# Kernel tuning notes

Hardware: AMD Instinct MI355X
Metric: run time of the kernel (lower is better)

Reference implementation:

```python
import jax, jax.numpy as jnp
import numpy as np

B, L, D = 1, 512, 1024
NH, NKV, NR = 16, 4, 16
HD, RD = 64, 64
NREP = NH // NKV  # 4
ATTN_SCALE = 1.0 / float(np.sqrt(HD))
REL_SCALE = 1.0 / float(np.sqrt(RD))


def setup_inputs() -> dict:
    key = jax.random.key(0)
    ks = jax.random.split(key, 9)
    x = jax.random.normal(ks[0], (B, L, D), jnp.float32)
    symbols = jax.random.normal(ks[1], (B, L, D), jnp.float32)
    # standard llama-style RoPE frequencies: [L, HD//2]
    inv_freq = 1.0 / (10000.0 ** (np.arange(0, HD, 2, dtype=np.float32) / HD))
    f = np.outer(np.arange(L, dtype=np.float32), inv_freq)
    freqs_cos = jnp.asarray(np.cos(f), jnp.float32)
    freqs_sin = jnp.asarray(np.sin(f), jnp.float32)
    s = 0.02
    wq_attn = jax.random.normal(ks[2], (D, NH * HD), jnp.float32) * s
    wk_attn = jax.random.normal(ks[3], (D, NKV * HD), jnp.float32) * s
    wq_rel = jax.random.normal(ks[4], (D, NR * RD), jnp.float32) * s
    wk_rel = jax.random.normal(ks[5], (D, NR * RD), jnp.float32) * s
    wr = jax.random.normal(ks[6], (NR, NH * HD), jnp.float32) * s
    wv = jax.random.normal(ks[7], (D, NKV * HD), jnp.float32) * s
    wo = jax.random.normal(ks[8], (NH * HD, NH * HD), jnp.float32) * s
    return dict(x=x, symbols=symbols, freqs_cos=freqs_cos, freqs_sin=freqs_sin,
                wq_attn=wq_attn, wk_attn=wk_attn, wq_rel=wq_rel, wk_rel=wk_rel,
                wr=wr, wv=wv, wo=wo)


def _rope(t, cos, sin):
    # t: [b, l, h, hd]; cos/sin: [l, hd//2]
    tr = t.reshape(t.shape[:-1] + (HD // 2, 2))
    re, im = tr[..., 0], tr[..., 1]
    c = cos[None, :, None, :]
    s = sin[None, :, None, :]
    out = jnp.stack([re * c - im * s, re * s + im * c], axis=-1)
    return out.reshape(t.shape)


def reference(x, symbols, freqs_cos, freqs_sin, wq_attn, wk_attn, wq_rel, wk_rel, wr, wv, wo):
    b, l, _ = x.shape
    q = (x @ wq_attn).reshape(b, l, NH, HD)
    k = (x @ wk_attn).reshape(b, l, NKV, HD)
    qr = (x @ wq_rel).reshape(b, l, NR, RD)
    kr = (x @ wk_rel).reshape(b, l, NR, RD)
    sv = (symbols @ wv).reshape(b, l, NKV, HD)
    q = _rope(q, freqs_cos, freqs_sin)
    k = _rope(k, freqs_cos, freqs_sin)
    # GQA: repeat kv heads consecutively (matches torch repeat_kv expand+reshape)
    k = jnp.repeat(k, NREP, axis=2)
    sv = jnp.repeat(sv, NREP, axis=2)
    scores = jnp.einsum('bihd,bjhd->bhij', q, k) * ATTN_SCALE
    causal = jnp.tril(jnp.ones((l, l), bool))
    scores = jnp.where(causal[None, None], scores, -jnp.inf)
    attn = jax.nn.softmax(scores, axis=-1)  # [b, nh, l, l]
    # relation scores, identity activation, laid out as [b, i, j, nr]
    relations = jnp.einsum('bird,bjrd->bijr', qr, kr) * REL_SCALE
    proj_rel = (relations @ wr).reshape(b, l, l, NH, HD)  # dominant intermediate
    attended_symbols = jnp.einsum('bhij,bjhd->bihd', attn, sv)
    attended_relations = jnp.einsum('bhij,bijhd->bihd', attn, proj_rel)
    out = (attended_symbols + attended_relations).reshape(b, l, NH * HD) @ wo
    return out, attn, relations
```

## Files before the change

kernel.cpp:

```cpp
#include <hip/hip_runtime.h>
#include <math.h>

#define ATTN_SCALE 0.125f
#define REL_SCALE 0.125f

using ushort = unsigned short;
using bf16x8 = __attribute__((ext_vector_type(8))) __bf16;
using floatx4 = __attribute__((ext_vector_type(4))) float;
using ushort8 = __attribute__((ext_vector_type(8))) ushort;
using ushort4v = __attribute__((ext_vector_type(4))) ushort;

__device__ __forceinline__ ushort f2bf(float x) {
  unsigned int u = __builtin_bit_cast(unsigned int, x);
  u += 0x7fffu + ((u >> 16) & 1u);
  return (ushort)(u >> 16);
}

__device__ __forceinline__ void mfma_body(const ushort* __restrict__ A, int lda,
                                          const ushort* __restrict__ Bt, int ldb,
                                          int K, floatx4 (&acc)[2][2]) {
  __shared__ ushort As[64][72];
  __shared__ ushort Bs[64][72];
  const int tid = threadIdx.x;
  const int sr = tid >> 2, sc = (tid & 3) << 4;
  const int lane = tid & 63;
  const int wy = (tid >> 7) & 1, wx = (tid >> 6) & 1;
  const int lm = lane & 15, lq = lane >> 4;
  const ushort* a_rd = &As[32 * wy + lm][lq * 8];
  const ushort* b_rd = &Bs[32 * wx + lm][lq * 8];
  for (int k0 = 0; k0 < K; k0 += 64) {
    const ushort* Ap = A + (size_t)sr * lda + k0 + sc;
    ushort8 av0 = *(const ushort8*)Ap;
    ushort8 av1 = *(const ushort8*)(Ap + 8);
    const ushort* Bp = Bt + (size_t)sr * ldb + k0 + sc;
    ushort8 bv0 = *(const ushort8*)Bp;
    ushort8 bv1 = *(const ushort8*)(Bp + 8);
    __syncthreads();
    *(ushort8*)&As[sr][sc] = av0;
    *(ushort8*)&As[sr][sc + 8] = av1;
    *(ushort8*)&Bs[sr][sc] = bv0;
    *(ushort8*)&Bs[sr][sc + 8] = bv1;
    __syncthreads();
#pragma unroll
    for (int kh = 0; kh < 2; ++kh) {
      bf16x8 a0 = *(const bf16x8*)(a_rd + kh * 32);
      bf16x8 a1 = *(const bf16x8*)(a_rd + 16 * 72 + kh * 32);
      bf16x8 b0 = *(const bf16x8*)(b_rd + kh * 32);
      bf16x8 b1 = *(const bf16x8*)(b_rd + 16 * 72 + kh * 32);
      acc[0][0] = __builtin_amdgcn_mfma_f32_16x16x32_bf16(a0, b0, acc[0][0], 0, 0, 0);
      acc[0][1] = __builtin_amdgcn_mfma_f32_16x16x32_bf16(a0, b1, acc[0][1], 0, 0, 0);
      acc[1][0] = __builtin_amdgcn_mfma_f32_16x16x32_bf16(a1, b0, acc[1][0], 0, 0, 0);
      acc[1][1] = __builtin_amdgcn_mfma_f32_16x16x32_bf16(a1, b1, acc[1][1], 0, 0, 0);
    }
  }
}

#define EPILOG_VARS                                                   \
  const int lane = threadIdx.x & 63;                                  \
  const int wy = (threadIdx.x >> 7) & 1, wx = (threadIdx.x >> 6) & 1; \
  const int lm = lane & 15, lq = lane >> 4;

__global__ __launch_bounds__(256) void prep_kernel(
    const float* __restrict__ x, const float* __restrict__ sym,
    const float* __restrict__ wq, const float* __restrict__ wk,
    const float* __restrict__ wqr, const float* __restrict__ wkr,
    const float* __restrict__ wv, const float* __restrict__ wo,
    ushort* __restrict__ xb, ushort* __restrict__ symb,
    ushort* __restrict__ wqT, ushort* __restrict__ wkT, ushort* __restrict__ wqrT,
    ushort* __restrict__ wkrT, ushort* __restrict__ wvT, ushort* __restrict__ woT) {
  if (blockIdx.z == 6) {
    int b = blockIdx.y * 32 + blockIdx.x;
    if (b >= 512) return;
    int idx = b * 256 + threadIdx.x;
    int i4 = idx << 2;
    float4 v = *(const float4*)(x + i4);
    uint2 o;
    o.x = (unsigned)f2bf(v.x) | ((unsigned)f2bf(v.y) << 16);
    o.y = (unsigned)f2bf(v.z) | ((unsigned)f2bf(v.w) << 16);
    *(uint2*)(xb + i4) = o;
    float4 w = *(const float4*)(sym + i4);
    o.x = (unsigned)f2bf(w.x) | ((unsigned)f2bf(w.y) << 16);
    o.y = (unsigned)f2bf(w.z) | ((unsigned)f2bf(w.w) << 16);
    *(uint2*)(symb + i4) = o;
    return;
  }
  __shared__ ushort t[32][33];
  const float* in;
  ushort* out;
  int N;
  switch (blockIdx.z) {
    case 0: in = wq;  out = wqT;  N = 1024; break;
    case 1: in = wk;  out = wkT;  N = 256;  break;
    case 2: in = wqr; out = wqrT; N = 1024; break;
    case 3: in = wkr; out = wkrT; N = 1024; break;
    case 4: in = wv;  out = wvT;  N = 256;  break;
    default: in = wo; out = woT;  N = 1024; break;
  }
  int n0 = blockIdx.x << 5;
  if (n0 >= N) return;
  int k0 = blockIdx.y << 5;
  int tx = threadIdx.x & 31, ty = threadIdx.x >> 5;
#pragma unroll
  for (int rr = 0; rr < 32; rr += 8)
    t[ty + rr][tx] = f2bf(in[(size_t)(k0 + ty + rr) * N + n0 + tx]);
  __syncthreads();
#pragma unroll
  for (int rr = 0; rr < 32; rr += 8)
    out[(size_t)(n0 + ty + rr) * 1024 + k0 + tx] = t[tx][ty + rr];
}

__global__ __launch_bounds__(256) void proj_mfma(
    const ushort* __restrict__ xb, const ushort* __restrict__ symb,
    const ushort* __restrict__ wqT, const ushort* __restrict__ wkT,
    const ushort* __restrict__ wqrT, const ushort* __restrict__ wkrT,
    const ushort* __restrict__ wvT,
    ushort* __restrict__ qb, ushort* __restrict__ kb, ushort* __restrict__ qrb,
    ushort* __restrict__ krb, ushort* __restrict__ svT,
    const float* __restrict__ fcos, const float* __restrict__ fsin) {
  const int z = blockIdx.z;
  const ushort* A = xb;
  const ushort* Bt;
  ushort* C;
  int N;
  switch (z) {
    case 0: Bt = wqT;  C = qb;  N = 1024; break;
    case 1: Bt = wkT;  C = kb;  N = 256;  break;
    case 2: Bt = wqrT; C = qrb; N = 1024; break;
    case 3: Bt = wkrT; C = krb; N = 1024; break;
    default: A = symb; Bt = wvT; C = svT; N = 256; break;
  }
  const int bn = blockIdx.x << 6;
  if (bn >= N) return;
  const int bm = blockIdx.y << 6;
  floatx4 acc[2][2] = {};
  mfma_body(A + (size_t)bm * 1024, 1024, Bt + (size_t)bn * 1024, 1024, 1024, acc);
  EPILOG_VARS
  if (z <= 1) {
#pragma unroll
    for (int sy = 0; sy < 2; ++sy)
#pragma unroll
      for (int sx = 0; sx < 2; ++sx)
#pragma unroll
        for (int e = 0; e < 4; ++e) {
          int row = bm + 32 * wy + 16 * sy + 4 * lq + e;
          int col = bn + 32 * wx + 16 * sx + lm;
          float v = acc[sy][sx][e];
          float pv = __shfl_xor(v, 1);
          int d = col & 63, p = d >> 1;
          float c = fcos[(row << 5) + p], s = fsin[(row << 5) + p];
          float o = (d & 1) ? fmaf(pv, s, v * c) : fmaf(v, c, -pv * s);
          C[(size_t)row * N + col] = f2bf(o);
        }
  } else if (z == 4) {
#pragma unroll
    for (int sy = 0; sy < 2; ++sy)
#pragma unroll
      for (int sx = 0; sx < 2; ++sx)
#pragma unroll
        for (int e = 0; e < 4; ++e) {
          int row = bm + 32 * wy + 16 * sy + 4 * lq + e;
          int col = bn + 32 * wx + 16 * sx + lm;
          svT[(size_t)col * 512 + row] = f2bf(acc[sy][sx][e]);
        }
  } else {
#pragma unroll
    for (int sy = 0; sy < 2; ++sy)
#pragma unroll
      for (int sx = 0; sx < 2; ++sx)
#pragma unroll
        for (int e = 0; e < 4; ++e) {
          int row = bm + 32 * wy + 16 * sy + 4 * lq + e;
          int col = bn + 32 * wx + 16 * sx + lm;
          C[(size_t)row * N + col] = f2bf(acc[sy][sx][e]);
        }
  }
}

__global__ __launch_bounds__(256) void relflash_kernel(
    const ushort* __restrict__ qb, const ushort* __restrict__ kb,
    const ushort* __restrict__ svT, const ushort* __restrict__ qrb,
    const ushort* __restrict__ krb, float* __restrict__ attn,
    float* __restrict__ asym, float* __restrict__ rel) {
  __shared__ float S[16][516];
  __shared__ ushort P[16][520];
  const int bx = blockIdx.x;
  const int tid = threadIdx.x, wave = tid >> 6, lane = tid & 63;
  const int lm = lane & 15, lq = lane >> 4;
  if (bx >= 512) {
    const int b = bx - 512;
    const int bi0 = (b >> 4) << 5, bj0 = (b & 15) << 5;
    const int ib = bi0 + ((wave >> 1) << 4), jb = bj0 + ((wave & 1) << 4);
    const ushort* qrow = qrb + (size_t)(ib + lm) * 1024 + lq * 8;
    const ushort* krow = krb + (size_t)(jb + lm) * 1024 + lq * 8;
#pragma unroll
    for (int rq = 0; rq < 4; ++rq) {
      floatx4 acc[4];
#pragma unroll
      for (int rr = 0; rr < 4; ++rr) {
        int roff = ((rq << 2) + rr) << 6;
        bf16x8 a0 = *(const bf16x8*)(qrow + roff);
        bf16x8 a1 = *(const bf16x8*)(qrow + roff + 32);
        bf16x8 b0 = *(const bf16x8*)(krow + roff);
        bf16x8 b1 = *(const bf16x8*)(krow + roff + 32);
        floatx4 t = {0.f, 0.f, 0.f, 0.f};
        t = __builtin_amdgcn_mfma_f32_16x16x32_bf16(a0, b0, t, 0, 0, 0);
        t = __builtin_amdgcn_mfma_f32_16x16x32_bf16(a1, b1, t, 0, 0, 0);
        acc[rr] = t;
      }
#pragma unroll
      for (int e = 0; e < 4; ++e) {
        int i = ib + 4 * lq + e, j = jb + lm;
        float4 v = make_float4(acc[0][e] * REL_SCALE, acc[1][e] * REL_SCALE,
                               acc[2][e] * REL_SCALE, acc[3][e] * REL_SCALE);
        *(float4*)(rel + ((size_t)i * 512 + j) * 16 + (rq << 2)) = v;
      }
    }
    return;
  }
  const int h = bx >> 5, it = 31 - (bx & 31);
  const int i0 = it << 4, kv = h >> 2;
  const int ntiles = it + 1;
  const ushort* qrow = qb + (size_t)(i0 + lm) * 1024 + (h << 6) + lq * 8;
  bf16x8 a0 = *(const bf16x8*)(qrow);
  bf16x8 a1 = *(const bf16x8*)(qrow + 32);
  for (int jt = wave; jt < ntiles; jt += 4) {
    int jb = jt << 4;
    const ushort* krow = kb + (size_t)(jb + lm) * 256 + (kv << 6) + lq * 8;
    bf16x8 b0 = *(const bf16x8*)(krow);
    bf16x8 b1 = *(const bf16x8*)(krow + 32);
    floatx4 acc = {0.f, 0.f, 0.f, 0.f};
    acc = __builtin_amdgcn_mfma_f32_16x16x32_bf16(a0, b0, acc, 0, 0, 0);
    acc = __builtin_amdgcn_mfma_f32_16x16x32_bf16(a1, b1, acc, 0, 0, 0);
#pragma unroll
    for (int e = 0; e < 4; ++e) S[4 * lq + e][jb + lm] = acc[e] * ATTN_SCALE;
  }
  __syncthreads();
  const int row = tid >> 4, t16 = tid & 15;
  const int i = i0 + row;
  const int nj = ntiles << 4;
  float m = -INFINITY;
  for (int s = 0; (s << 6) < nj; ++s) {
    int j4 = (t16 << 2) + (s << 6);
    float4 v = *(const float4*)&S[row][j4];
    if (j4 + 0 <= i) m = fmaxf(m, v.x);
    if (j4 + 1 <= i) m = fmaxf(m, v.y);
    if (j4 + 2 <= i) m = fmaxf(m, v.z);
    if (j4 + 3 <= i) m = fmaxf(m, v.w);
  }
#pragma unroll
  for (int o = 8; o; o >>= 1) m = fmaxf(m, __shfl_xor(m, o, 16));
  float sum = 0.f;
  for (int s = 0; (s << 6) < nj; ++s) {
    int j4 = (t16 << 2) + (s << 6);
    float4 v = *(const float4*)&S[row][j4];
    if (j4 + 0 <= i) sum += __expf(v.x - m);
    if (j4 + 1 <= i) sum += __expf(v.y - m);
    if (j4 + 2 <= i) sum += __expf(v.z - m);
    if (j4 + 3 <= i) sum += __expf(v.w - m);
  }
#pragma unroll
  for (int o = 8; o; o >>= 1) sum += __shfl_xor(sum, o, 16);
  const float inv = 1.f / sum;
  float* arow = attn + (size_t)h * 262144 + (size_t)i * 512;
  for (int s = 0; s < 8; ++s) {
    int j4 = (t16 << 2) + (s << 6);
    float4 o4 = {0.f, 0.f, 0.f, 0.f};
    if (j4 < nj) {
      float4 v = *(const float4*)&S[row][j4];
      o4.x = (j4 + 0 <= i) ? __expf(v.x - m) * inv : 0.f;
      o4.y = (j4 + 1 <= i) ? __expf(v.y - m) * inv : 0.f;
      o4.z = (j4 + 2 <= i) ? __expf(v.z - m) * inv : 0.f;
      o4.w = (j4 + 3 <= i) ? __expf(v.w - m) * inv : 0.f;
    }
    *(float4*)(arow + j4) = o4;
    ushort4v p4;
    p4.x = f2bf(o4.x); p4.y = f2bf(o4.y); p4.z = f2bf(o4.z); p4.w = f2bf(o4.w);
    *(ushort4v*)&P[row][j4] = p4;
  }
  __syncthreads();
  const int dbase = wave << 4;
  floatx4 acc2 = {0.f, 0.f, 0.f, 0.f};
  const ushort* svrow = svT + (size_t)((kv << 6) + dbase + lm) * 512;
  const int kmax = (nj + 31) & ~31;
  for (int kt = 0; kt < kmax; kt += 32) {
    bf16x8 pa = *(const bf16x8*)&P[lm][kt + lq * 8];
    bf16x8 pb = *(const bf16x8*)(svrow + kt + lq * 8);
    acc2 = __builtin_amdgcn_mfma_f32_16x16x32_bf16(pa, pb, acc2, 0, 0, 0);
  }
#pragma unroll
  for (int e = 0; e < 4; ++e)
    asym[(size_t)(i0 + 4 * lq + e) * 1024 + (h << 6) + dbase + lm] = acc2[e];
}

__global__ __launch_bounds__(256) void tker_combine(const float* __restrict__ attn,
                                                    const float* __restrict__ rel,
                                                    const float* __restrict__ asym,
                                                    const float* __restrict__ wr,
                                                    ushort* __restrict__ attb) {
  const int i = blockIdx.x, tid = threadIdx.x;
  __shared__ float a_s[16][132];
  __shared__ float r_s[16][132];
  __shared__ float Ts[16][17];
  const int h = tid >> 4, r = tid & 15;
  float acc = 0.f;
  for (int j0 = 0; j0 <= i; j0 += 128) {
#pragma unroll
    for (int idx = tid; idx < 512; idx += 256) {
      int hh = idx >> 5, j4 = (idx & 31) << 2;
      *(float4*)&a_s[hh][j4] =
          *(const float4*)(attn + (size_t)hh * 262144 + (size_t)i * 512 + j0 + j4);
    }
#pragma unroll
    for (int idx = tid; idx < 512; idx += 256) {
      int j = idx >> 2, r4 = (idx & 3) << 2;
      float4 v = *(const float4*)(rel + ((size_t)i * 512 + j0 + j) * 16 + r4);
      r_s[r4 + 0][j] = v.x;
      r_s[r4 + 1][j] = v.y;
      r_s[r4 + 2][j] = v.z;
      r_s[r4 + 3][j] = v.w;
    }
    __syncthreads();
#pragma unroll
    for (int jj = 0; jj < 128; jj += 4) {
      float4 a4 = *(const float4*)&a_s[h][jj];
      float4 r4v = *(const float4*)&r_s[r][jj];
      acc = fmaf(a4.x, r4v.x, acc);
      acc = fmaf(a4.y, r4v.y, acc);
      acc = fmaf(a4.z, r4v.z, acc);
      acc = fmaf(a4.w, r4v.w, acc);
    }
    __syncthreads();
  }
  Ts[h][r] = acc;
  __syncthreads();
  const int hc = tid >> 4, d4 = (tid & 15) << 2;
  float4 o = *(const float4*)(asym + (size_t)i * 1024 + (hc << 6) + d4);
#pragma unroll
  for (int rr = 0; rr < 16; ++rr) {
    float tv = Ts[hc][rr];
    float4 w4 = *(const float4*)(wr + (size_t)rr * 1024 + (hc << 6) + d4);
    o.x = fmaf(tv, w4.x, o.x);
    o.y = fmaf(tv, w4.y, o.y);
    o.z = fmaf(tv, w4.z, o.z);
    o.w = fmaf(tv, w4.w, o.w);
  }
  ushort4v ob;
  ob.x = f2bf(o.x); ob.y = f2bf(o.y); ob.z = f2bf(o.z); ob.w = f2bf(o.w);
  *(ushort4v*)(attb + (size_t)i * 1024 + (hc << 6) + d4) = ob;
}

__global__ __launch_bounds__(256) void out_mfma(const ushort* __restrict__ attb,
                                                const ushort* __restrict__ woT,
                                                float* __restrict__ out) {
  __shared__ ushort As[64][72];
  __shared__ ushort Bs[32][72];
  const int bn = blockIdx.x << 5, bm = blockIdx.y << 6;
  const int tid = threadIdx.x;
  const int sr = tid >> 2, sc = (tid & 3) << 4;
  const int br = tid >> 3, bc = (tid & 7) << 3;
  const int lane = tid & 63;
  const int wy = (tid >> 7) & 1, wx = (tid >> 6) & 1;
  const int lm = lane & 15, lq = lane >> 4;
  const ushort* a_rd = &As[32 * wy + lm][lq * 8];
  const ushort* b_rd = &Bs[16 * wx + lm][lq * 8];
  floatx4 acc[2] = {};
  for (int k0 = 0; k0 < 1024; k0 += 64) {
    const ushort* Ap = attb + (size_t)(bm + sr) * 1024 + k0 + sc;
    ushort8 av0 = *(const ushort8*)Ap;
    ushort8 av1 = *(const ushort8*)(Ap + 8);
    ushort8 bv = *(const ushort8*)(woT + (size_t)(bn + br) * 1024 + k0 + bc);
    __syncthreads();
    *(ushort8*)&As[sr][sc] = av0;
    *(ushort8*)&As[sr][sc + 8] = av1;
    *(ushort8*)&Bs[br][bc] = bv;
    __syncthreads();
#pragma unroll
    for (int kh = 0; kh < 2; ++kh) {
      bf16x8 a0 = *(const bf16x8*)(a_rd + kh * 32);
      bf16x8 a1 = *(const bf16x8*)(a_rd + 16 * 72 + kh * 32);
      bf16x8 b0 = *(const bf16x8*)(b_rd + kh * 32);
      acc[0] = __builtin_amdgcn_mfma_f32_16x16x32_bf16(a0, b0, acc[0], 0, 0, 0);
      acc[1] = __builtin_amdgcn_mfma_f32_16x16x32_bf16(a1, b0, acc[1], 0, 0, 0);
    }
  }
#pragma unroll
  for (int sy = 0; sy < 2; ++sy)
#pragma unroll
    for (int e = 0; e < 4; ++e) {
      int row = bm + 32 * wy + 16 * sy + 4 * lq + e;
      int col = bn + 16 * wx + lm;
      out[(size_t)row * 1024 + col] = acc[sy][e];
    }
}

extern "C" void kernel_launch(void* const* d_in, const int* in_sizes, int n_in,
                              void* d_out, int out_size, void* d_ws, size_t ws_size,
                              hipStream_t stream) {
  const float* x       = (const float*)d_in[0];
  const float* symbols = (const float*)d_in[1];
  const float* fcos    = (const float*)d_in[2];
  const float* fsin    = (const float*)d_in[3];
  const float* wq_attn = (const float*)d_in[4];
  const float* wk_attn = (const float*)d_in[5];
  const float* wq_rel  = (const float*)d_in[6];
  const float* wk_rel  = (const float*)d_in[7];
  const float* wr      = (const float*)d_in[8];
  const float* wv      = (const float*)d_in[9];
  const float* wo      = (const float*)d_in[10];

  float* out  = (float*)d_out;
  float* attn = out + 524288;
  float* rel  = attn + 4194304;

  char* wsb = (char*)d_ws;
  const size_t MB = 1 << 20;
  ushort* xb   = (ushort*)(wsb);
  ushort* symb = (ushort*)(wsb + 1 * MB);
  ushort* wqT  = (ushort*)(wsb + 2 * MB);
  ushort* wkT  = (ushort*)(wsb + 4 * MB);
  ushort* wqrT = (ushort*)(wsb + 4 * MB + 512 * 1024);
  ushort* wkrT = (ushort*)(wsb + 6 * MB + 512 * 1024);
  ushort* wvT  = (ushort*)(wsb + 8 * MB + 512 * 1024);
  ushort* woT  = (ushort*)(wsb + 9 * MB);
  ushort* qb   = (ushort*)(wsb + 11 * MB);
  ushort* kb   = (ushort*)(wsb + 12 * MB);
  ushort* qrb  = (ushort*)(wsb + 12 * MB + 256 * 1024);
  ushort* krb  = (ushort*)(wsb + 13 * MB + 256 * 1024);
  ushort* svT  = (ushort*)(wsb + 14 * MB + 256 * 1024);
  float*  asym = (float*)(wsb + 2 * MB);
  ushort* attb = (ushort*)(wsb + 4 * MB + 512 * 1024);

  prep_kernel<<<dim3(32, 32, 7), 256, 0, stream>>>(x, symbols, wq_attn, wk_attn,
                                                   wq_rel, wk_rel, wv, wo,
                                                   xb, symb, wqT, wkT, wqrT, wkrT, wvT, woT);
  proj_mfma<<<dim3(16, 8, 5), 256, 0, stream>>>(xb, symb, wqT, wkT, wqrT, wkrT, wvT,
                                                qb, kb, qrb, krb, svT, fcos, fsin);
  relflash_kernel<<<dim3(768), 256, 0, stream>>>(qb, kb, svT, qrb, krb, attn, asym, rel);
  tker_combine<<<dim3(512), 256, 0, stream>>>(attn, rel, asym, wr, attb);
  out_mfma<<<dim3(32, 8), 256, 0, stream>>>(attb, woT, out);
}
```

Measured before the change: 153.8 us.

## Fuse fp32-to-bf16 conversion and weight transpose into GEMM loads; cache softmax exps

```diff
diff --git a/kernel.cpp b/kernel.cpp
--- a/kernel.cpp
+++ b/kernel.cpp
@@ -16,30 +16,64 @@
   return (ushort)(u >> 16);
 }
 
-__device__ __forceinline__ void mfma_body(const ushort* __restrict__ A, int lda,
-                                          const ushort* __restrict__ Bt, int ldb,
-                                          int K, floatx4 (&acc)[2][2]) {
+__global__ __launch_bounds__(256) void proj_mfma(
+    const float* __restrict__ x, const float* __restrict__ symbols,
+    const float* __restrict__ wq, const float* __restrict__ wk,
+    const float* __restrict__ wqr, const float* __restrict__ wkr,
+    const float* __restrict__ wv,
+    ushort* __restrict__ qb, ushort* __restrict__ kb, ushort* __restrict__ qrb,
+    ushort* __restrict__ krb, ushort* __restrict__ svT,
+    const float* __restrict__ fcos, const float* __restrict__ fsin) {
   __shared__ ushort As[64][72];
   __shared__ ushort Bs[64][72];
+  const int z = blockIdx.z;
+  const float* A = x;
+  const float* W;
+  ushort* C;
+  int N;
+  switch (z) {
+    case 0: W = wq;  C = qb;  N = 1024; break;
+    case 1: W = wk;  C = kb;  N = 256;  break;
+    case 2: W = wqr; C = qrb; N = 1024; break;
+    case 3: W = wkr; C = krb; N = 1024; break;
+    default: A = symbols; W = wv; C = svT; N = 256; break;
+  }
+  const int bn = blockIdx.x << 6;
+  if (bn >= N) return;
+  const int bm = blockIdx.y << 6;
   const int tid = threadIdx.x;
   const int sr = tid >> 2, sc = (tid & 3) << 4;
+  const int kk = tid >> 4, nl = (tid & 15) << 2;
   const int lane = tid & 63;
   const int wy = (tid >> 7) & 1, wx = (tid >> 6) & 1;
   const int lm = lane & 15, lq = lane >> 4;
   const ushort* a_rd = &As[32 * wy + lm][lq * 8];
   const ushort* b_rd = &Bs[32 * wx + lm][lq * 8];
-  for (int k0 = 0; k0 < K; k0 += 64) {
-    const ushort* Ap = A + (size_t)sr * lda + k0 + sc;
-    ushort8 av0 = *(const ushort8*)Ap;
-    ushort8 av1 = *(const ushort8*)(Ap + 8);
-    const ushort* Bp = Bt + (size_t)sr * ldb + k0 + sc;
-    ushort8 bv0 = *(const ushort8*)Bp;
-    ushort8 bv1 = *(const ushort8*)(Bp + 8);
+  floatx4 acc[2][2] = {};
+  for (int k0 = 0; k0 < 1024; k0 += 64) {
+    const float* Ap = A + (size_t)(bm + sr) * 1024 + k0 + sc;
+    float4 f0 = *(const float4*)(Ap);
+    float4 f1 = *(const float4*)(Ap + 4);
+    float4 f2 = *(const float4*)(Ap + 8);
+    float4 f3 = *(const float4*)(Ap + 12);
+    ushort8 av0 = ushort8{f2bf(f0.x), f2bf(f0.y), f2bf(f0.z), f2bf(f0.w),
+                          f2bf(f1.x), f2bf(f1.y), f2bf(f1.z), f2bf(f1.w)};
+    ushort8 av1 = ushort8{f2bf(f2.x), f2bf(f2.y), f2bf(f2.z), f2bf(f2.w),
+                          f2bf(f3.x), f2bf(f3.y), f2bf(f3.z), f2bf(f3.w)};
+    float4 bw[4];
+#pragma unroll
+    for (int p = 0; p < 4; ++p)
+      bw[p] = *(const float4*)(W + (size_t)(k0 + kk + 16 * p) * N + bn + nl);
     __syncthreads();
     *(ushort8*)&As[sr][sc] = av0;
     *(ushort8*)&As[sr][sc + 8] = av1;
-    *(ushort8*)&Bs[sr][sc] = bv0;
-    *(ushort8*)&Bs[sr][sc + 8] = bv1;
+#pragma unroll
+    for (int p = 0; p < 4; ++p) {
+      Bs[nl + 0][kk + 16 * p] = f2bf(bw[p].x);
+      Bs[nl + 1][kk + 16 * p] = f2bf(bw[p].y);
+      Bs[nl + 2][kk + 16 * p] = f2bf(bw[p].z);
+      Bs[nl + 3][kk + 16 * p] = f2bf(bw[p].w);
+    }
     __syncthreads();
 #pragma unroll
     for (int kh = 0; kh < 2; ++kh) {
@@ -53,88 +87,6 @@
       acc[1][1] = __builtin_amdgcn_mfma_f32_16x16x32_bf16(a1, b1, acc[1][1], 0, 0, 0);
     }
   }
-}
-
-#define EPILOG_VARS                                                   \
-  const int lane = threadIdx.x & 63;                                  \
-  const int wy = (threadIdx.x >> 7) & 1, wx = (threadIdx.x >> 6) & 1; \
-  const int lm = lane & 15, lq = lane >> 4;
-
-__global__ __launch_bounds__(256) void prep_kernel(
-    const float* __restrict__ x, const float* __restrict__ sym,
-    const float* __restrict__ wq, const float* __restrict__ wk,
-    const float* __restrict__ wqr, const float* __restrict__ wkr,
-    const float* __restrict__ wv, const float* __restrict__ wo,
-    ushort* __restrict__ xb, ushort* __restrict__ symb,
-    ushort* __restrict__ wqT, ushort* __restrict__ wkT, ushort* __restrict__ wqrT,
-    ushort* __restrict__ wkrT, ushort* __restrict__ wvT, ushort* __restrict__ woT) {
-  if (blockIdx.z == 6) {
-    int b = blockIdx.y * 32 + blockIdx.x;
-    if (b >= 512) return;
-    int idx = b * 256 + threadIdx.x;
-    int i4 = idx << 2;
-    float4 v = *(const float4*)(x + i4);
-    uint2 o;
-    o.x = (unsigned)f2bf(v.x) | ((unsigned)f2bf(v.y) << 16);
-    o.y = (unsigned)f2bf(v.z) | ((unsigned)f2bf(v.w) << 16);
-    *(uint2*)(xb + i4) = o;
-    float4 w = *(const float4*)(sym + i4);
-    o.x = (unsigned)f2bf(w.x) | ((unsigned)f2bf(w.y) << 16);
-    o.y = (unsigned)f2bf(w.z) | ((unsigned)f2bf(w.w) << 16);
-    *(uint2*)(symb + i4) = o;
-    return;
-  }
-  __shared__ ushort t[32][33];
-  const float* in;
-  ushort* out;
-  int N;
-  switch (blockIdx.z) {
-    case 0: in = wq;  out = wqT;  N = 1024; break;
-    case 1: in = wk;  out = wkT;  N = 256;  break;
-    case 2: in = wqr; out = wqrT; N = 1024; break;
-    case 3: in = wkr; out = wkrT; N = 1024; break;
-    case 4: in = wv;  out = wvT;  N = 256;  break;
-    default: in = wo; out = woT;  N = 1024; break;
-  }
-  int n0 = blockIdx.x << 5;
-  if (n0 >= N) return;
-  int k0 = blockIdx.y << 5;
-  int tx = threadIdx.x & 31, ty = threadIdx.x >> 5;
-#pragma unroll
-  for (int rr = 0; rr < 32; rr += 8)
-    t[ty + rr][tx] = f2bf(in[(size_t)(k0 + ty + rr) * N + n0 + tx]);
-  __syncthreads();
-#pragma unroll
-  for (int rr = 0; rr < 32; rr += 8)
-    out[(size_t)(n0 + ty + rr) * 1024 + k0 + tx] = t[tx][ty + rr];
-}
-
-__global__ __launch_bounds__(256) void proj_mfma(
-    const ushort* __restrict__ xb, const ushort* __restrict__ symb,
-    const ushort* __restrict__ wqT, const ushort* __restrict__ wkT,
-    const ushort* __restrict__ wqrT, const ushort* __restrict__ wkrT,
-    const ushort* __restrict__ wvT,
-    ushort* __restrict__ qb, ushort* __restrict__ kb, ushort* __restrict__ qrb,
-    ushort* __restrict__ krb, ushort* __restrict__ svT,
-    const float* __restrict__ fcos, const float* __restrict__ fsin) {
-  const int z = blockIdx.z;
-  const ushort* A = xb;
-  const ushort* Bt;
-  ushort* C;
-  int N;
-  switch (z) {
-    case 0: Bt = wqT;  C = qb;  N = 1024; break;
-    case 1: Bt = wkT;  C = kb;  N = 256;  break;
-    case 2: Bt = wqrT; C = qrb; N = 1024; break;
-    case 3: Bt = wkrT; C = krb; N = 1024; break;
-    default: A = symb; Bt = wvT; C = svT; N = 256; break;
-  }
-  const int bn = blockIdx.x << 6;
-  if (bn >= N) return;
-  const int bm = blockIdx.y << 6;
-  floatx4 acc[2][2] = {};
-  mfma_body(A + (size_t)bm * 1024, 1024, Bt + (size_t)bn * 1024, 1024, 1024, acc);
-  EPILOG_VARS
   if (z <= 1) {
 #pragma unroll
     for (int sy = 0; sy < 2; ++sy)
@@ -253,10 +205,12 @@
   for (int s = 0; (s << 6) < nj; ++s) {
     int j4 = (t16 << 2) + (s << 6);
     float4 v = *(const float4*)&S[row][j4];
-    if (j4 + 0 <= i) sum += __expf(v.x - m);
-    if (j4 + 1 <= i) sum += __expf(v.y - m);
-    if (j4 + 2 <= i) sum += __expf(v.z - m);
-    if (j4 + 3 <= i) sum += __expf(v.w - m);
+    v.x = (j4 + 0 <= i) ? __expf(v.x - m) : 0.f;
+    v.y = (j4 + 1 <= i) ? __expf(v.y - m) : 0.f;
+    v.z = (j4 + 2 <= i) ? __expf(v.z - m) : 0.f;
+    v.w = (j4 + 3 <= i) ? __expf(v.w - m) : 0.f;
+    sum += v.x + v.y + v.z + v.w;
+    *(float4*)&S[row][j4] = v;
   }
 #pragma unroll
   for (int o = 8; o; o >>= 1) sum += __shfl_xor(sum, o, 16);
@@ -267,10 +221,10 @@
     float4 o4 = {0.f, 0.f, 0.f, 0.f};
     if (j4 < nj) {
       float4 v = *(const float4*)&S[row][j4];
-      o4.x = (j4 + 0 <= i) ? __expf(v.x - m) * inv : 0.f;
-      o4.y = (j4 + 1 <= i) ? __expf(v.y - m) * inv : 0.f;
-      o4.z = (j4 + 2 <= i) ? __expf(v.z - m) * inv : 0.f;
-      o4.w = (j4 + 3 <= i) ? __expf(v.w - m) * inv : 0.f;
+      o4.x = v.x * inv;
+      o4.y = v.y * inv;
+      o4.z = v.z * inv;
+      o4.w = v.w * inv;
     }
     *(float4*)(arow + j4) = o4;
     ushort4v p4;
@@ -350,14 +304,14 @@
 }
 
 __global__ __launch_bounds__(256) void out_mfma(const ushort* __restrict__ attb,
-                                                const ushort* __restrict__ woT,
+                                                const float* __restrict__ wo,
                                                 float* __restrict__ out) {
   __shared__ ushort As[64][72];
   __shared__ ushort Bs[32][72];
   const int bn = blockIdx.x << 5, bm = blockIdx.y << 6;
   const int tid = threadIdx.x;
   const int sr = tid >> 2, sc = (tid & 3) << 4;
-  const int br = tid >> 3, bc = (tid & 7) << 3;
+  const int kk = tid >> 3, nl = (tid & 7) << 2;
   const int lane = tid & 63;
   const int wy = (tid >> 7) & 1, wx = (tid >> 6) & 1;
   const int lm = lane & 15, lq = lane >> 4;
@@ -368,11 +322,20 @@
     const ushort* Ap = attb + (size_t)(bm + sr) * 1024 + k0 + sc;
     ushort8 av0 = *(const ushort8*)Ap;
     ushort8 av1 = *(const ushort8*)(Ap + 8);
-    ushort8 bv = *(const ushort8*)(woT + (size_t)(bn + br) * 1024 + k0 + bc);
+    float4 bw[2];
+#pragma unroll
+    for (int p = 0; p < 2; ++p)
+      bw[p] = *(const float4*)(wo + (size_t)(k0 + kk + 32 * p) * 1024 + bn + nl);
     __syncthreads();
     *(ushort8*)&As[sr][sc] = av0;
     *(ushort8*)&As[sr][sc + 8] = av1;
-    *(ushort8*)&Bs[br][bc] = bv;
+#pragma unroll
+    for (int p = 0; p < 2; ++p) {
+      Bs[nl + 0][kk + 32 * p] = f2bf(bw[p].x);
+      Bs[nl + 1][kk + 32 * p] = f2bf(bw[p].y);
+      Bs[nl + 2][kk + 32 * p] = f2bf(bw[p].z);
+      Bs[nl + 3][kk + 32 * p] = f2bf(bw[p].w);
+    }
     __syncthreads();
 #pragma unroll
     for (int kh = 0; kh < 2; ++kh) {
@@ -413,29 +376,19 @@
   float* rel  = attn + 4194304;
 
   char* wsb = (char*)d_ws;
-  const size_t MB = 1 << 20;
-  ushort* xb   = (ushort*)(wsb);
-  ushort* symb = (ushort*)(wsb + 1 * MB);
-  ushort* wqT  = (ushort*)(wsb + 2 * MB);
-  ushort* wkT  = (ushort*)(wsb + 4 * MB);
-  ushort* wqrT = (ushort*)(wsb + 4 * MB + 512 * 1024);
-  ushort* wkrT = (ushort*)(wsb + 6 * MB + 512 * 1024);
-  ushort* wvT  = (ushort*)(wsb + 8 * MB + 512 * 1024);
-  ushort* woT  = (ushort*)(wsb + 9 * MB);
-  ushort* qb   = (ushort*)(wsb + 11 * MB);
-  ushort* kb   = (ushort*)(wsb + 12 * MB);
-  ushort* qrb  = (ushort*)(wsb + 12 * MB + 256 * 1024);
-  ushort* krb  = (ushort*)(wsb + 13 * MB + 256 * 1024);
-  ushort* svT  = (ushort*)(wsb + 14 * MB + 256 * 1024);
-  float*  asym = (float*)(wsb + 2 * MB);
-  ushort* attb = (ushort*)(wsb + 4 * MB + 512 * 1024);
-
-  prep_kernel<<<dim3(32, 32, 7), 256, 0, stream>>>(x, symbols, wq_attn, wk_attn,
-                                                   wq_rel, wk_rel, wv, wo,
-                                                   xb, symb, wqT, wkT, wqrT, wkrT, wvT, woT);
-  proj_mfma<<<dim3(16, 8, 5), 256, 0, stream>>>(xb, symb, wqT, wkT, wqrT, wkrT, wvT,
+  const size_t KB = 1024;
+  ushort* qb   = (ushort*)(wsb);
+  ushort* kb   = (ushort*)(wsb + 1024 * KB);
+  ushort* qrb  = (ushort*)(wsb + 1280 * KB);
+  ushort* krb  = (ushort*)(wsb + 2304 * KB);
+  ushort* svT  = (ushort*)(wsb + 3328 * KB);
+  float*  asym = (float*)(wsb + 3584 * KB);
+  ushort* attb = (ushort*)(wsb + 5632 * KB);
+
+  proj_mfma<<<dim3(16, 8, 5), 256, 0, stream>>>(x, symbols, wq_attn, wk_attn,
+                                                wq_rel, wk_rel, wv,
                                                 qb, kb, qrb, krb, svT, fcos, fsin);
   relflash_kernel<<<dim3(768), 256, 0, stream>>>(qb, kb, svT, qrb, krb, attn, asym, rel);
   tker_combine<<<dim3(512), 256, 0, stream>>>(attn, rel, asym, wr, attb);
-  out_mfma<<<dim3(32, 8), 256, 0, stream>>>(attb, woT, out);
-}
+  out_mfma<<<dim3(32, 8), 256, 0, stream>>>(attb, wo, out);
+}
```

Result: slower. 169.5 us (+10.2%).

## Compute attention-relation contraction with MFMA using transposed bf16 relation copy

Applied to the files above, without the earlier changes.

```diff
diff --git a/kernel.cpp b/kernel.cpp
--- a/kernel.cpp
+++ b/kernel.cpp
@@ -180,7 +180,8 @@
     const ushort* __restrict__ qb, const ushort* __restrict__ kb,
     const ushort* __restrict__ svT, const ushort* __restrict__ qrb,
     const ushort* __restrict__ krb, float* __restrict__ attn,
-    float* __restrict__ asym, float* __restrict__ rel) {
+    float* __restrict__ asym, float* __restrict__ rel,
+    ushort* __restrict__ rel_bT) {
   __shared__ float S[16][516];
   __shared__ ushort P[16][520];
   const int bx = blockIdx.x;
@@ -213,6 +214,11 @@
         float4 v = make_float4(acc[0][e] * REL_SCALE, acc[1][e] * REL_SCALE,
                                acc[2][e] * REL_SCALE, acc[3][e] * REL_SCALE);
         *(float4*)(rel + ((size_t)i * 512 + j) * 16 + (rq << 2)) = v;
+        size_t tb = (size_t)i * 8192 + (size_t)(rq << 2) * 512 + j;
+        rel_bT[tb]         = f2bf(v.x);
+        rel_bT[tb + 512]   = f2bf(v.y);
+        rel_bT[tb + 1024]  = f2bf(v.z);
+        rel_bT[tb + 1536]  = f2bf(v.w);
       }
     }
     return;
@@ -253,10 +259,12 @@
   for (int s = 0; (s << 6) < nj; ++s) {
     int j4 = (t16 << 2) + (s << 6);
     float4 v = *(const float4*)&S[row][j4];
-    if (j4 + 0 <= i) sum += __expf(v.x - m);
-    if (j4 + 1 <= i) sum += __expf(v.y - m);
-    if (j4 + 2 <= i) sum += __expf(v.z - m);
-    if (j4 + 3 <= i) sum += __expf(v.w - m);
+    v.x = (j4 + 0 <= i) ? __expf(v.x - m) : 0.f;
+    v.y = (j4 + 1 <= i) ? __expf(v.y - m) : 0.f;
+    v.z = (j4 + 2 <= i) ? __expf(v.z - m) : 0.f;
+    v.w = (j4 + 3 <= i) ? __expf(v.w - m) : 0.f;
+    sum += v.x + v.y + v.z + v.w;
+    *(float4*)&S[row][j4] = v;
   }
 #pragma unroll
   for (int o = 8; o; o >>= 1) sum += __shfl_xor(sum, o, 16);
@@ -267,10 +275,10 @@
     float4 o4 = {0.f, 0.f, 0.f, 0.f};
     if (j4 < nj) {
       float4 v = *(const float4*)&S[row][j4];
-      o4.x = (j4 + 0 <= i) ? __expf(v.x - m) * inv : 0.f;
-      o4.y = (j4 + 1 <= i) ? __expf(v.y - m) * inv : 0.f;
-      o4.z = (j4 + 2 <= i) ? __expf(v.z - m) * inv : 0.f;
-      o4.w = (j4 + 3 <= i) ? __expf(v.w - m) * inv : 0.f;
+      o4.x = v.x * inv;
+      o4.y = v.y * inv;
+      o4.z = v.z * inv;
+      o4.w = v.w * inv;
     }
     *(float4*)(arow + j4) = o4;
     ushort4v p4;
@@ -293,60 +301,56 @@
 }
 
 __global__ __launch_bounds__(256) void tker_combine(const float* __restrict__ attn,
-                                                    const float* __restrict__ rel,
+                                                    const ushort* __restrict__ rel_bT,
                                                     const float* __restrict__ asym,
                                                     const float* __restrict__ wr,
                                                     ushort* __restrict__ attb) {
-  const int i = blockIdx.x, tid = threadIdx.x;
-  __shared__ float a_s[16][132];
-  __shared__ float r_s[16][132];
-  __shared__ float Ts[16][17];
-  const int h = tid >> 4, r = tid & 15;
-  float acc = 0.f;
-  for (int j0 = 0; j0 <= i; j0 += 128) {
-#pragma unroll
-    for (int idx = tid; idx < 512; idx += 256) {
-      int hh = idx >> 5, j4 = (idx & 31) << 2;
-      *(float4*)&a_s[hh][j4] =
-          *(const float4*)(attn + (size_t)hh * 262144 + (size_t)i * 512 + j0 + j4);
-    }
-#pragma unroll
-    for (int idx = tid; idx < 512; idx += 256) {
-      int j = idx >> 2, r4 = (idx & 3) << 2;
-      float4 v = *(const float4*)(rel + ((size_t)i * 512 + j0 + j) * 16 + r4);
-      r_s[r4 + 0][j] = v.x;
-      r_s[r4 + 1][j] = v.y;
-      r_s[r4 + 2][j] = v.z;
-      r_s[r4 + 3][j] = v.w;
-    }
-    __syncthreads();
-#pragma unroll
-    for (int jj = 0; jj < 128; jj += 4) {
-      float4 a4 = *(const float4*)&a_s[h][jj];
-      float4 r4v = *(const float4*)&r_s[r][jj];
-      acc = fmaf(a4.x, r4v.x, acc);
-      acc = fmaf(a4.y, r4v.y, acc);
-      acc = fmaf(a4.z, r4v.z, acc);
-      acc = fmaf(a4.w, r4v.w, acc);
-    }
-    __syncthreads();
-  }
-  Ts[h][r] = acc;
+  const int i0 = blockIdx.x << 2;
+  const int tid = threadIdx.x, wave = tid >> 6, lane = tid & 63;
+  const int lm = lane & 15, lq = lane >> 4;
+  const int i = i0 + wave;
+  __shared__ float Ts[4][16][17];
+  floatx4 acc = {0.f, 0.f, 0.f, 0.f};
+  const float* arow = attn + (size_t)lm * 262144 + (size_t)i * 512;
+  const ushort* brow = rel_bT + (size_t)i * 8192 + (size_t)lm * 512;
+  const int ktiles = (i >> 5) + 1;
+  for (int kt = 0; kt < ktiles; ++kt) {
+    int k = (kt << 5) + lq * 8;
+    float4 f0 = *(const float4*)(arow + k);
+    float4 f1 = *(const float4*)(arow + k + 4);
+    bf16x8 a = __builtin_bit_cast(bf16x8,
+        ushort8{f2bf(f0.x), f2bf(f0.y), f2bf(f0.z), f2bf(f0.w),
+                f2bf(f1.x), f2bf(f1.y), f2bf(f1.z), f2bf(f1.w)});
+    bf16x8 b = *(const bf16x8*)(brow + k);
+    acc = __builtin_amdgcn_mfma_f32_16x16x32_bf16(a, b, acc, 0, 0, 0);
+  }
+#pragma unroll
+  for (int e = 0; e < 4; ++e) Ts[wave][4 * lq + e][lm] = acc[e];
   __syncthreads();
   const int hc = tid >> 4, d4 = (tid & 15) << 2;
-  float4 o = *(const float4*)(asym + (size_t)i * 1024 + (hc << 6) + d4);
+  float4 o[4];
+#pragma unroll
+  for (int iw = 0; iw < 4; ++iw)
+    o[iw] = *(const float4*)(asym + (size_t)(i0 + iw) * 1024 + (hc << 6) + d4);
 #pragma unroll
   for (int rr = 0; rr < 16; ++rr) {
-    float tv = Ts[hc][rr];
     float4 w4 = *(const float4*)(wr + (size_t)rr * 1024 + (hc << 6) + d4);
-    o.x = fmaf(tv, w4.x, o.x);
-    o.y = fmaf(tv, w4.y, o.y);
-    o.z = fmaf(tv, w4.z, o.z);
-    o.w = fmaf(tv, w4.w, o.w);
-  }
-  ushort4v ob;
-  ob.x = f2bf(o.x); ob.y = f2bf(o.y); ob.z = f2bf(o.z); ob.w = f2bf(o.w);
-  *(ushort4v*)(attb + (size_t)i * 1024 + (hc << 6) + d4) = ob;
+#pragma unroll
+    for (int iw = 0; iw < 4; ++iw) {
+      float tv = Ts[iw][hc][rr];
+      o[iw].x = fmaf(tv, w4.x, o[iw].x);
+      o[iw].y = fmaf(tv, w4.y, o[iw].y);
+      o[iw].z = fmaf(tv, w4.z, o[iw].z);
+      o[iw].w = fmaf(tv, w4.w, o[iw].w);
+    }
+  }
+#pragma unroll
+  for (int iw = 0; iw < 4; ++iw) {
+    ushort4v ob;
+    ob.x = f2bf(o[iw].x); ob.y = f2bf(o[iw].y);
+    ob.z = f2bf(o[iw].z); ob.w = f2bf(o[iw].w);
+    *(ushort4v*)(attb + (size_t)(i0 + iw) * 1024 + (hc << 6) + d4) = ob;
+  }
 }
 
 __global__ __launch_bounds__(256) void out_mfma(const ushort* __restrict__ attb,
@@ -413,29 +417,31 @@
   float* rel  = attn + 4194304;
 
   char* wsb = (char*)d_ws;
-  const size_t MB = 1 << 20;
-  ushort* xb   = (ushort*)(wsb);
-  ushort* symb = (ushort*)(wsb + 1 * MB);
-  ushort* wqT  = (ushort*)(wsb + 2 * MB);
-  ushort* wkT  = (ushort*)(wsb + 4 * MB);
-  ushort* wqrT = (ushort*)(wsb + 4 * MB + 512 * 1024);
-  ushort* wkrT = (ushort*)(wsb + 6 * MB + 512 * 1024);
-  ushort* wvT  = (ushort*)(wsb + 8 * MB + 512 * 1024);
-  ushort* woT  = (ushort*)(wsb + 9 * MB);
-  ushort* qb   = (ushort*)(wsb + 11 * MB);
-  ushort* kb   = (ushort*)(wsb + 12 * MB);
-  ushort* qrb  = (ushort*)(wsb + 12 * MB + 256 * 1024);
-  ushort* krb  = (ushort*)(wsb + 13 * MB + 256 * 1024);
-  ushort* svT  = (ushort*)(wsb + 14 * MB + 256 * 1024);
-  float*  asym = (float*)(wsb + 2 * MB);
-  ushort* attb = (ushort*)(wsb + 4 * MB + 512 * 1024);
+  const size_t KB = 1024;
+  ushort* xb     = (ushort*)(wsb);
+  ushort* symb   = (ushort*)(wsb + 1024 * KB);
+  ushort* wqT    = (ushort*)(wsb + 2048 * KB);
+  ushort* wkT    = (ushort*)(wsb + 4096 * KB);
+  ushort* wqrT   = (ushort*)(wsb + 4608 * KB);
+  ushort* wkrT   = (ushort*)(wsb + 6656 * KB);
+  ushort* wvT    = (ushort*)(wsb + 8704 * KB);
+  ushort* woT    = (ushort*)(wsb + 9216 * KB);
+  ushort* qb     = (ushort*)(wsb + 11264 * KB);
+  ushort* kb     = (ushort*)(wsb + 12288 * KB);
+  ushort* qrb    = (ushort*)(wsb + 12544 * KB);
+  ushort* krb    = (ushort*)(wsb + 13568 * KB);
+  ushort* svT    = (ushort*)(wsb + 14592 * KB);
+  float*  asym   = (float*)(wsb + 14848 * KB);
+  ushort* attb   = (ushort*)(wsb + 16896 * KB);
+  ushort* rel_bT = (ushort*)(wsb + 17920 * KB);
 
   prep_kernel<<<dim3(32, 32, 7), 256, 0, stream>>>(x, symbols, wq_attn, wk_attn,
                                                    wq_rel, wk_rel, wv, wo,
                                                    xb, symb, wqT, wkT, wqrT, wkrT, wvT, woT);
   proj_mfma<<<dim3(16, 8, 5), 256, 0, stream>>>(xb, symb, wqT, wkT, wqrT, wkrT, wvT,
                                                 qb, kb, qrb, krb, svT, fcos, fsin);
-  relflash_kernel<<<dim3(768), 256, 0, stream>>>(qb, kb, svT, qrb, krb, attn, asym, rel);
-  tker_combine<<<dim3(512), 256, 0, stream>>>(attn, rel, asym, wr, attb);
+  relflash_kernel<<<dim3(768), 256, 0, stream>>>(qb, kb, svT, qrb, krb, attn, asym,
+                                                 rel, rel_bT);
+  tker_combine<<<dim3(128), 256, 0, stream>>>(attn, rel_bT, asym, wr, attb);
   out_mfma<<<dim3(32, 8), 256, 0, stream>>>(attb, woT, out);
 }
```

Result: no change. 152.9 us (-0.6%).
